# Kernel tuning notes

Measured on AMD Instinct MI355X. Metric: run time of the kernel, lower is better.

## Reference

```python
import jax, jax.numpy as jnp
import numpy as np

CLASS_NUM = 80
NUM_PRED = 2
TOPK = 1000
LEVEL_SIZES = [147456, 36864, 9216, 2304, 576]


def _make_anchors(key, n):
    k1, k2, k3, k4 = jax.random.split(key, 4)
    x1 = jax.random.uniform(k1, (n,)) * 1000.0
    y1 = jax.random.uniform(k2, (n,)) * 1000.0
    w = jax.random.uniform(k3, (n,)) * 200.0 + 8.0
    h = jax.random.uniform(k4, (n,)) * 200.0 + 8.0
    return jnp.stack([x1, y1, x1 + w, y1 + h], axis=1)


def setup_inputs() -> dict:
    key = jax.random.key(0)
    inp = {}
    for i, n in enumerate(LEVEL_SIZES):
        ka = jax.random.fold_in(key, 3 * i)
        kc = jax.random.fold_in(key, 3 * i + 1)
        kr = jax.random.fold_in(key, 3 * i + 2)
        inp[f"anchors{i}"] = _make_anchors(ka, n)
        inp[f"cls{i}"] = jax.random.normal(kc, (1, n, CLASS_NUM * NUM_PRED), dtype=jnp.float32)
        inp[f"reg{i}"] = jax.random.normal(kr, (1, n, 4 * NUM_PRED), dtype=jnp.float32) * 0.1
    return inp


def bbox_transform_inv(anchors, deltas):
    # anchors: [N,4] (x1,y1,x2,y2); deltas: [N,4] (dx,dy,dw,dh)
    w = anchors[:, 2] - anchors[:, 0] + 1.0
    h = anchors[:, 3] - anchors[:, 1] + 1.0
    cx = anchors[:, 0] + 0.5 * w
    cy = anchors[:, 1] + 0.5 * h
    pcx = cx + deltas[:, 0] * w
    pcy = cy + deltas[:, 1] * h
    pw = w * jnp.exp(deltas[:, 2])
    ph = h * jnp.exp(deltas[:, 3])
    return jnp.stack([pcx - 0.5 * pw, pcy - 0.5 * ph,
                      pcx + 0.5 * pw, pcy + 0.5 * ph], axis=1)


def _per_layer_inference(anchors_list, cls_list, reg_list):
    keep_a, keep_c, keep_r = [], [], []
    for a, c, r in zip(anchors_list, cls_list, reg_list):
        a = a.reshape(-1, 4)
        c = c[0].reshape(-1, CLASS_NUM * NUM_PRED)
        r = r[0].reshape(-1, 4 * NUM_PRED)
        if a.shape[0] > TOPK:
            ruler = jnp.max(c, axis=1)
            _, inds = jax.lax.top_k(ruler, TOPK)
            a, c, r = a[inds], c[inds], r[inds]
        keep_a.append(a)
        keep_c.append(jax.nn.sigmoid(c))
        keep_r.append(r)
    a = jnp.concatenate(keep_a, axis=0)   # [N,4]
    c = jnp.concatenate(keep_c, axis=0)   # [N, C*P]
    r = jnp.concatenate(keep_r, axis=0)   # [N, 4*P]
    n = a.shape[0]
    tag = (jnp.arange(CLASS_NUM, dtype=a.dtype) + 1.0)
    tag = jnp.tile(tag[None, :], (n, 1)).reshape(-1, 1)  # [N*C,1]
    scores0 = c[:, :CLASS_NUM].reshape(-1, 1)
    scores1 = c[:, CLASS_NUM:].reshape(-1, 1)
    bbox0 = bbox_transform_inv(a, r[:, :4])
    bbox1 = bbox_transform_inv(a, r[:, 4:])
    bbox0 = jnp.tile(bbox0, (1, CLASS_NUM)).reshape(-1, 4)
    bbox1 = jnp.tile(bbox1, (1, CLASS_NUM)).reshape(-1, 4)
    pred0 = jnp.concatenate([bbox0, scores0, tag], axis=1)
    pred1 = jnp.concatenate([bbox1, scores1, tag], axis=1)
    return jnp.concatenate([pred0, pred1], axis=1)  # [N*C, 12]


def reference(anchors0, anchors1, anchors2, anchors3, anchors4,
              cls0, cls1, cls2, cls3, cls4,
              reg0, reg1, reg2, reg3, reg4):
    return _per_layer_inference(
        [anchors0, anchors1, anchors2, anchors3, anchors4],
        [cls0, cls1, cls2, cls3, cls4],
        [reg0, reg1, reg2, reg3, reg4])
```

## Files before the change

kernel.cpp:

```cpp
#include <hip/hip_runtime.h>

#define CLS   160
#define TOPKN 1000
#define N0 147456
#define N1 36864
#define N2 9216
#define N3 2304
#define N4 576
#define NROWS (N0 + N1 + N2 + N3)
#define BD1 N0
#define BD2 (N0 + N1)
#define BD3 (N0 + N1 + N2)
#define NSEL (4 * TOPKN + N4)
#define NBINS 65536
#define CAND_CAP 2048

__device__ __forceinline__ unsigned sortable(float f) {
    unsigned u = __float_as_uint(f);
    return (u & 0x80000000u) ? ~u : (u | 0x80000000u);
}

__global__ __launch_bounds__(256) void k_ruler(
    const float* __restrict__ c0, const float* __restrict__ c1,
    const float* __restrict__ c2, const float* __restrict__ c3,
    unsigned* __restrict__ keys, unsigned* __restrict__ hist)
{
    int tid = blockIdx.x * 256 + threadIdx.x;
    if (tid < 4 * NBINS + 4096) hist[tid] = 0;

    int r0 = blockIdx.x << 7;
    const float* cb; int lr0;
    if (r0 < BD1)      { cb = c0; lr0 = r0; }
    else if (r0 < BD2) { cb = c1; lr0 = r0 - BD1; }
    else if (r0 < BD3) { cb = c2; lr0 = r0 - BD2; }
    else               { cb = c3; lr0 = r0 - BD3; }

    int wv   = threadIdx.x >> 6;
    int lane = threadIdx.x & 63;
    int sub  = lane >> 3;
    int col  = lane & 7;
    #pragma unroll
    for (int i = 0; i < 4; ++i) {
        int rrel = wv * 32 + i * 8 + sub;
        const float4* p = (const float4*)cb + (size_t)(lr0 + rrel) * 40 + col;
        float m = -3.4e38f;
        #pragma unroll
        for (int k = 0; k < 5; ++k) {
            float4 v = p[8 * k];
            m = fmaxf(m, fmaxf(fmaxf(v.x, v.y), fmaxf(v.z, v.w)));
        }
        m = fmaxf(m, __shfl_xor(m, 1));
        m = fmaxf(m, __shfl_xor(m, 2));
        m = fmaxf(m, __shfl_xor(m, 4));
        if (col == 0) keys[r0 + rrel] = sortable(m);
    }
}

__global__ __launch_bounds__(256) void k_hist(const unsigned* __restrict__ keys,
                                              unsigned* __restrict__ hist,
                                              unsigned* __restrict__ coarse)
{
    int b        = blockIdx.x;
    int level    = b >> 8;
    unsigned seg = (b >> 4) & 15;
    int chunk    = b & 15;
    __shared__ unsigned cnt[4096];
    for (int i = threadIdx.x; i < 4096; i += 256) cnt[i] = 0;
    __syncthreads();
    int base, n;
    switch (level) {
        case 0:  base = 0;   n = N0; break;
        case 1:  base = BD1; n = N1; break;
        case 2:  base = BD2; n = N2; break;
        default: base = BD3; n = N3; break;
    }
    int q = n >> 4;
    const uint4* kp = (const uint4*)(keys + base + chunk * q);
    int nv = q >> 2;
    for (int i = threadIdx.x; i < nv; i += 256) {
        uint4 k = kp[i];
        unsigned b0 = k.x >> 16, b1 = k.y >> 16, b2 = k.z >> 16, b3 = k.w >> 16;
        if ((b0 >> 12) == seg) atomicAdd(&cnt[b0 & 4095u], 1u);
        if ((b1 >> 12) == seg) atomicAdd(&cnt[b1 & 4095u], 1u);
        if ((b2 >> 12) == seg) atomicAdd(&cnt[b2 & 4095u], 1u);
        if ((b3 >> 12) == seg) atomicAdd(&cnt[b3 & 4095u], 1u);
    }
    __syncthreads();
    unsigned* h = hist + level * NBINS + (seg << 12);
    for (int i = threadIdx.x; i < 4096; i += 256) {
        unsigned c = cnt[i];
        if (c) atomicAdd(&h[i], c);
    }
    if (threadIdx.x < 64) {
        int j = threadIdx.x;
        unsigned s2 = 0;
        #pragma unroll 8
        for (int i = 0; i < 64; ++i) s2 += cnt[j * 64 + ((i + j) & 63)];
        if (s2) atomicAdd(&coarse[level * 1024 + (int)(seg << 6) + j], s2);
    }
}

__global__ __launch_bounds__(1024) void k_select(const unsigned* __restrict__ keys,
                                                 const unsigned* __restrict__ hist,
                                                 const unsigned* __restrict__ coarse,
                                                 unsigned* __restrict__ sel)
{
    int level = blockIdx.x;
    int t     = threadIdx.x;
    int lane  = t & 63;
    const unsigned* h = hist + level * NBINS;

    __shared__ unsigned s[1024];
    __shared__ unsigned long long a[CAND_CAP];
    __shared__ unsigned thr_s, cnt_s, chunk_s, cum0_s;

    s[t] = coarse[level * 1024 + t];
    if (t == 0) cnt_s = 0;
    __syncthreads();
    for (int off = 1; off < 1024; off <<= 1) {
        unsigned v   = s[t];
        unsigned add = (t + off < 1024) ? s[t + off] : 0u;
        __syncthreads();
        s[t] = v + add;
        __syncthreads();
    }
    if (s[t] >= TOPKN && (t == 1023 || s[t + 1] < TOPKN)) {
        chunk_s = (unsigned)t;
        cum0_s  = (t == 1023) ? 0u : s[t + 1];
    }
    __syncthreads();
    if (t < 64) {
        unsigned c = h[chunk_s * 64 + (unsigned)t];
        unsigned suf = c;
        #pragma unroll
        for (int off = 1; off < 64; off <<= 1) {
            unsigned v = __shfl_down(suf, off);
            if (t + off < 64) suf += v;
        }
        unsigned long long mask = __ballot(cum0_s + suf >= TOPKN);
        if (t == 0)
            thr_s = (chunk_s * 64 + (63 - (unsigned)__clzll(mask))) << 16;
    }
    __syncthreads();
    unsigned thr = thr_s;

    int base, n;
    switch (level) {
        case 0:  base = 0;   n = N0; break;
        case 1:  base = BD1; n = N1; break;
        case 2:  base = BD2; n = N2; break;
        default: base = BD3; n = N3; break;
    }
    const uint4* kp = (const uint4*)(keys + base);
    int nv = n >> 2;
    for (int i = t; i < nv; i += 1024) {
        uint4 k4 = kp[i];
        unsigned kv[4] = {k4.x, k4.y, k4.z, k4.w};
        #pragma unroll
        for (int c = 0; c < 4; ++c) {
            bool pass = kv[c] >= thr;
            unsigned long long mask = __ballot(pass);
            if (pass) {
                int leader    = __ffsll((long long)mask) - 1;
                unsigned tot  = (unsigned)__popcll(mask);
                unsigned rank = (unsigned)__popcll(mask & ((1ull << lane) - 1ull));
                unsigned bp = 0;
                if (lane == leader) bp = atomicAdd(&cnt_s, tot);
                bp = (unsigned)__shfl((int)bp, leader);
                unsigned pos = bp + rank;
                if (pos < CAND_CAP)
                    a[pos] = ((unsigned long long)kv[c] << 32) |
                             (unsigned)~(unsigned)(4 * i + c);
            }
        }
    }
    __syncthreads();
    unsigned cnt = cnt_s;
    if (cnt > CAND_CAP) cnt = CAND_CAP;

    for (int i = t; i < (int)cnt; i += 1024) {
        unsigned long long mine = a[i];
        unsigned rank = 0;
        for (int j = 0; j < (int)cnt; ++j) rank += (a[j] > mine) ? 1u : 0u;
        if (rank < TOPKN)
            sel[level * TOPKN + rank] = ~(unsigned)(mine & 0xFFFFFFFFull);
    }
}

__global__ __launch_bounds__(256) void k_epilogue(
    const float* a0, const float* a1, const float* a2, const float* a3, const float* a4,
    const float* c0, const float* c1, const float* c2, const float* c3, const float* c4,
    const float* r0, const float* r1, const float* r2, const float* r3, const float* r4,
    const unsigned* __restrict__ sel, float* __restrict__ out)
{
    int s = blockIdx.x;
    int level, idx;
    if (s < 4 * TOPKN) {
        level = s / TOPKN;
        idx   = (int)sel[s];
    } else {
        level = 4;
        idx   = s - 4 * TOPKN;
    }
    const float *A, *C, *R;
    switch (level) {
        case 0: A = a0; C = c0; R = r0; break;
        case 1: A = a1; C = c1; R = r1; break;
        case 2: A = a2; C = c2; R = r2; break;
        case 3: A = a3; C = c3; R = r3; break;
        default: A = a4; C = c4; R = r4; break;
    }

    __shared__ float sc[CLS];
    __shared__ float bb[8];

    const float* cp = C + (size_t)idx * CLS;
    if (threadIdx.x < CLS) {
        float x = cp[threadIdx.x];
        sc[threadIdx.x] = 1.0f / (1.0f + __expf(-x));
    }
    if (threadIdx.x == 192) {
        const float* ap = A + (size_t)idx * 4;
        const float* rp = R + (size_t)idx * 8;
        float x1 = ap[0], y1 = ap[1], x2 = ap[2], y2 = ap[3];
        float w  = x2 - x1 + 1.0f, h = y2 - y1 + 1.0f;
        float cx = x1 + 0.5f * w,  cy = y1 + 0.5f * h;
        #pragma unroll
        for (int p = 0; p < 2; ++p) {
            float pcx = cx + rp[4 * p + 0] * w;
            float pcy = cy + rp[4 * p + 1] * h;
            float pw  = w * __expf(rp[4 * p + 2]);
            float ph  = h * __expf(rp[4 * p + 3]);
            bb[4 * p + 0] = pcx - 0.5f * pw;
            bb[4 * p + 1] = pcy - 0.5f * ph;
            bb[4 * p + 2] = pcx + 0.5f * pw;
            bb[4 * p + 3] = pcy + 0.5f * ph;
        }
    }
    __syncthreads();

    float4* orow = (float4*)(out + (size_t)s * 960);
    if (threadIdx.x < 240) {
        int j = threadIdx.x / 3, part = threadIdx.x % 3;
        float tag = (float)(j + 1);
        float4 v;
        if (part == 0)      v = make_float4(bb[0], bb[1], bb[2], bb[3]);
        else if (part == 1) v = make_float4(sc[j], tag, bb[4], bb[5]);
        else                v = make_float4(bb[6], bb[7], sc[80 + j], tag);
        orow[threadIdx.x] = v;
    }
}

extern "C" void kernel_launch(void* const* d_in, const int* in_sizes, int n_in,
                              void* d_out, int out_size, void* d_ws, size_t ws_size,
                              hipStream_t stream)
{
    bool interleaved = (in_sizes[1] > 1000000);
    const float *A[5], *C[5], *R[5];
    for (int i = 0; i < 5; ++i) {
        if (interleaved) {
            A[i] = (const float*)d_in[3 * i + 0];
            C[i] = (const float*)d_in[3 * i + 1];
            R[i] = (const float*)d_in[3 * i + 2];
        } else {
            A[i] = (const float*)d_in[i];
            C[i] = (const float*)d_in[5 + i];
            R[i] = (const float*)d_in[10 + i];
        }
    }

    unsigned* keys   = (unsigned*)d_ws;
    unsigned* hist   = keys + NROWS;
    unsigned* coarse = hist + 4 * NBINS;
    unsigned* sel    = coarse + 4 * 1024;

    k_ruler<<<1530, 256, 0, stream>>>(C[0], C[1], C[2], C[3], keys, hist);
    k_hist<<<1024, 256, 0, stream>>>(keys, hist, coarse);
    k_select<<<4, 1024, 0, stream>>>(keys, hist, coarse, sel);
    k_epilogue<<<NSEL, 256, 0, stream>>>(A[0], A[1], A[2], A[3], A[4],
                                         C[0], C[1], C[2], C[3], C[4],
                                         R[0], R[1], R[2], R[3], R[4],
                                         sel, (float*)d_out);
}
```

Baseline: 82.41 us.

## Split top-k selection into parallel compaction and separate rank kernel

The single 4-block select kernel is split into a 64-block compaction kernel, with 16 slices per level that scan keys against the threshold and append candidates to global memory through global atomics, and a separate 4-block rank kernel. This spreads the key scan across more compute units instead of 4 blocks. In exchange it adds a kernel launch, global atomics and a global round trip for candidates. Each compaction block also recomputes the threshold scan redundantly.

```diff
diff --git a/kernel.cpp b/kernel.cpp
--- a/kernel.cpp
+++ b/kernel.cpp
@@ -26,7 +26,7 @@
     unsigned* __restrict__ keys, unsigned* __restrict__ hist)
 {
     int tid = blockIdx.x * 256 + threadIdx.x;
-    if (tid < 4 * NBINS + 4096) hist[tid] = 0;
+    if (tid < 4 * NBINS + 4096 + 8) hist[tid] = 0;
 
     int r0 = blockIdx.x << 7;
     const float* cb; int lr0;
@@ -100,22 +100,21 @@
     }
 }
 
-__global__ __launch_bounds__(1024) void k_select(const unsigned* __restrict__ keys,
-                                                 const unsigned* __restrict__ hist,
-                                                 const unsigned* __restrict__ coarse,
-                                                 unsigned* __restrict__ sel)
-{
-    int level = blockIdx.x;
+__global__ __launch_bounds__(1024) void k_compact(const unsigned* __restrict__ keys,
+                                                  const unsigned* __restrict__ hist,
+                                                  const unsigned* __restrict__ coarse,
+                                                  unsigned* __restrict__ ctrl,
+                                                  uint2* __restrict__ cand)
+{
+    int level = blockIdx.x >> 4;
+    int slice = blockIdx.x & 15;
     int t     = threadIdx.x;
     int lane  = t & 63;
-    const unsigned* h = hist + level * NBINS;
 
     __shared__ unsigned s[1024];
-    __shared__ unsigned long long a[CAND_CAP];
-    __shared__ unsigned thr_s, cnt_s, chunk_s, cum0_s;
+    __shared__ unsigned thr_s, chunk_s, cum0_s;
 
     s[t] = coarse[level * 1024 + t];
-    if (t == 0) cnt_s = 0;
     __syncthreads();
     for (int off = 1; off < 1024; off <<= 1) {
         unsigned v   = s[t];
@@ -130,29 +129,26 @@
     }
     __syncthreads();
     if (t < 64) {
+        const unsigned* h = hist + level * NBINS;
         unsigned c = h[chunk_s * 64 + (unsigned)t];
-        unsigned suf = c;
+        unsigned sufw = c;
         #pragma unroll
         for (int off = 1; off < 64; off <<= 1) {
-            unsigned v = __shfl_down(suf, off);
-            if (t + off < 64) suf += v;
-        }
-        unsigned long long mask = __ballot(cum0_s + suf >= TOPKN);
+            unsigned v = __shfl_down(sufw, off);
+            if (t + off < 64) sufw += v;
+        }
+        unsigned long long mask = __ballot(cum0_s + sufw >= TOPKN);
         if (t == 0)
             thr_s = (chunk_s * 64 + (63 - (unsigned)__clzll(mask))) << 16;
     }
     __syncthreads();
     unsigned thr = thr_s;
 
-    int base, n;
-    switch (level) {
-        case 0:  base = 0;   n = N0; break;
-        case 1:  base = BD1; n = N1; break;
-        case 2:  base = BD2; n = N2; break;
-        default: base = BD3; n = N3; break;
-    }
-    const uint4* kp = (const uint4*)(keys + base);
-    int nv = n >> 2;
+    int base = (level == 0) ? 0 : (level == 1) ? BD1 : (level == 2) ? BD2 : BD3;
+    int n    = (level == 0) ? N0 : (level == 1) ? N1 : (level == 2) ? N2 : N3;
+    int ns = n >> 4;
+    const uint4* kp = (const uint4*)(keys + base + slice * ns);
+    int nv = ns >> 2;
     for (int i = t; i < nv; i += 1024) {
         uint4 k4 = kp[i];
         unsigned kv[4] = {k4.x, k4.y, k4.z, k4.w};
@@ -165,20 +161,31 @@
                 unsigned tot  = (unsigned)__popcll(mask);
                 unsigned rank = (unsigned)__popcll(mask & ((1ull << lane) - 1ull));
                 unsigned bp = 0;
-                if (lane == leader) bp = atomicAdd(&cnt_s, tot);
+                if (lane == leader) bp = atomicAdd(&ctrl[4 + level], tot);
                 bp = (unsigned)__shfl((int)bp, leader);
                 unsigned pos = bp + rank;
                 if (pos < CAND_CAP)
-                    a[pos] = ((unsigned long long)kv[c] << 32) |
-                             (unsigned)~(unsigned)(4 * i + c);
+                    cand[level * CAND_CAP + pos] =
+                        make_uint2(kv[c], (unsigned)(slice * ns + 4 * i + c));
             }
         }
     }
-    __syncthreads();
-    unsigned cnt = cnt_s;
+}
+
+__global__ __launch_bounds__(1024) void k_rank(const uint2* __restrict__ cand,
+                                               const unsigned* __restrict__ ctrl,
+                                               unsigned* __restrict__ sel)
+{
+    int level = blockIdx.x;
+    unsigned cnt = ctrl[4 + level];
     if (cnt > CAND_CAP) cnt = CAND_CAP;
-
-    for (int i = t; i < (int)cnt; i += 1024) {
+    __shared__ unsigned long long a[CAND_CAP];
+    for (int i = threadIdx.x; i < (int)cnt; i += 1024) {
+        uint2 c = cand[level * CAND_CAP + i];
+        a[i] = ((unsigned long long)c.x << 32) | (unsigned)(~c.y);
+    }
+    __syncthreads();
+    for (int i = threadIdx.x; i < (int)cnt; i += 1024) {
         unsigned long long mine = a[i];
         unsigned rank = 0;
         for (int j = 0; j < (int)cnt; ++j) rank += (a[j] > mine) ? 1u : 0u;
@@ -272,11 +279,14 @@
     unsigned* keys   = (unsigned*)d_ws;
     unsigned* hist   = keys + NROWS;
     unsigned* coarse = hist + 4 * NBINS;
-    unsigned* sel    = coarse + 4 * 1024;
+    unsigned* ctrl   = coarse + 4096;
+    uint2*    cand   = (uint2*)(ctrl + 8);
+    unsigned* sel    = (unsigned*)(cand + 4 * CAND_CAP);
 
     k_ruler<<<1530, 256, 0, stream>>>(C[0], C[1], C[2], C[3], keys, hist);
     k_hist<<<1024, 256, 0, stream>>>(keys, hist, coarse);
-    k_select<<<4, 1024, 0, stream>>>(keys, hist, coarse, sel);
+    k_compact<<<64, 1024, 0, stream>>>(keys, hist, coarse, ctrl, cand);
+    k_rank<<<4, 1024, 0, stream>>>(cand, ctrl, sel);
     k_epilogue<<<NSEL, 256, 0, stream>>>(A[0], A[1], A[2], A[3], A[4],
                                          C[0], C[1], C[2], C[3], C[4],
                                          R[0], R[1], R[2], R[3], R[4],
```

New measurement: 90.08 us. 1.09x slower.

## Fuse histogram, select and epilogue into one persistent kernel with grid barriers

Applied to the files above, without the earlier changes.

Replaces the histogram, select and epilogue kernels with a single 64-block persistent kernel. Blocks keep their key slice in registers, build a 10-bit coarse histogram with wave-aggregated atomics, then refine only the winning coarse bin, so the large 64K-bin histogram and its zeroing are gone. Candidate selection is spread across 16 slices per level and cross-block progress uses spin-wait counters in global memory. The level-4 and top-k epilogue rows are handled by four teams inside each block. The aim is to cut launch overhead and the cost of the large histogram, in exchange for less parallelism in the epilogue, grid-barrier spin latency, and a reliance on all 64 blocks being resident at once.

```diff
diff --git a/kernel.cpp b/kernel.cpp
--- a/kernel.cpp
+++ b/kernel.cpp
@@ -12,8 +12,21 @@
 #define BD2 (N0 + N1)
 #define BD3 (N0 + N1 + N2)
 #define NSEL (4 * TOPKN + N4)
-#define NBINS 65536
 #define CAND_CAP 2048
+#define KMAX 9
+
+struct KP {
+    const float *A0, *A1, *A2, *A3, *A4;
+    const float *C0, *C1, *C2, *C3, *C4;
+    const float *R0, *R1, *R2, *R3, *R4;
+    unsigned *keys;
+    unsigned *coarse;
+    unsigned *fine_g;
+    unsigned *ctl;
+    unsigned long long *cand;
+    unsigned *sel;
+    float *out;
+};
 
 __device__ __forceinline__ unsigned sortable(float f) {
     unsigned u = __float_as_uint(f);
@@ -23,10 +36,10 @@
 __global__ __launch_bounds__(256) void k_ruler(
     const float* __restrict__ c0, const float* __restrict__ c1,
     const float* __restrict__ c2, const float* __restrict__ c3,
-    unsigned* __restrict__ keys, unsigned* __restrict__ hist)
+    unsigned* __restrict__ keys, unsigned* __restrict__ zbuf)
 {
     int tid = blockIdx.x * 256 + threadIdx.x;
-    if (tid < 4 * NBINS + 4096) hist[tid] = 0;
+    if (tid < 4480) zbuf[tid] = 0;
 
     int r0 = blockIdx.x << 7;
     const float* cb; int lr0;
@@ -56,66 +69,106 @@
     }
 }
 
-__global__ __launch_bounds__(256) void k_hist(const unsigned* __restrict__ keys,
-                                              unsigned* __restrict__ hist,
-                                              unsigned* __restrict__ coarse)
+__global__ __launch_bounds__(1024) void k_mega(KP p)
 {
-    int b        = blockIdx.x;
-    int level    = b >> 8;
-    unsigned seg = (b >> 4) & 15;
-    int chunk    = b & 15;
-    __shared__ unsigned cnt[4096];
-    for (int i = threadIdx.x; i < 4096; i += 256) cnt[i] = 0;
-    __syncthreads();
-    int base, n;
-    switch (level) {
-        case 0:  base = 0;   n = N0; break;
-        case 1:  base = BD1; n = N1; break;
-        case 2:  base = BD2; n = N2; break;
-        default: base = BD3; n = N3; break;
-    }
-    int q = n >> 4;
-    const uint4* kp = (const uint4*)(keys + base + chunk * q);
-    int nv = q >> 2;
-    for (int i = threadIdx.x; i < nv; i += 256) {
-        uint4 k = kp[i];
-        unsigned b0 = k.x >> 16, b1 = k.y >> 16, b2 = k.z >> 16, b3 = k.w >> 16;
-        if ((b0 >> 12) == seg) atomicAdd(&cnt[b0 & 4095u], 1u);
-        if ((b1 >> 12) == seg) atomicAdd(&cnt[b1 & 4095u], 1u);
-        if ((b2 >> 12) == seg) atomicAdd(&cnt[b2 & 4095u], 1u);
-        if ((b3 >> 12) == seg) atomicAdd(&cnt[b3 & 4095u], 1u);
-    }
-    __syncthreads();
-    unsigned* h = hist + level * NBINS + (seg << 12);
-    for (int i = threadIdx.x; i < 4096; i += 256) {
-        unsigned c = cnt[i];
-        if (c) atomicAdd(&h[i], c);
-    }
-    if (threadIdx.x < 64) {
-        int j = threadIdx.x;
-        unsigned s2 = 0;
-        #pragma unroll 8
-        for (int i = 0; i < 64; ++i) s2 += cnt[j * 64 + ((i + j) & 63)];
-        if (s2) atomicAdd(&coarse[level * 1024 + (int)(seg << 6) + j], s2);
-    }
-}
-
-__global__ __launch_bounds__(1024) void k_select(const unsigned* __restrict__ keys,
-                                                 const unsigned* __restrict__ hist,
-                                                 const unsigned* __restrict__ coarse,
-                                                 unsigned* __restrict__ sel)
-{
-    int level = blockIdx.x;
-    int t     = threadIdx.x;
-    int lane  = t & 63;
-    const unsigned* h = hist + level * NBINS;
+    const int b = blockIdx.x, lvl = b >> 4, slice = b & 15;
+    const int t = threadIdx.x, lane = t & 63;
+    const int team = t >> 8, tt = t & 255;
 
     __shared__ unsigned s[1024];
+    __shared__ unsigned fine[64];
     __shared__ unsigned long long a[CAND_CAP];
-    __shared__ unsigned thr_s, cnt_s, chunk_s, cum0_s;
-
-    s[t] = coarse[level * 1024 + t];
-    if (t == 0) cnt_s = 0;
+    __shared__ float sc[4][CLS];
+    __shared__ float bbx[4][8];
+    __shared__ unsigned thr_s, blockcnt, gbase_s, Cstar_s, cum0_s;
+
+    const int lbase = (lvl == 0) ? 0 : (lvl == 1) ? BD1 : (lvl == 2) ? BD2 : BD3;
+    const int ln    = (lvl == 0) ? N0 : (lvl == 1) ? N1 : (lvl == 2) ? N2 : N3;
+    const int ns    = ln >> 4;
+    const unsigned* kp = p.keys + lbase + slice * ns;
+
+    unsigned* done1 = p.ctl + 0;
+    unsigned* done2 = p.ctl + 4;
+    unsigned* done3 = p.ctl + 8;
+    unsigned* done4 = p.ctl + 12;
+    unsigned* cntp  = p.ctl + 32 + 16 * lvl;
+
+    s[t] = 0;
+    if (t == 0) blockcnt = 0;
+    __syncthreads();
+
+    unsigned kreg[KMAX];
+    #pragma unroll
+    for (int j = 0; j < KMAX; ++j) {
+        int li = j * 1024 + t;
+        kreg[j] = (li < ns) ? kp[li] : 0u;
+    }
+    #pragma unroll
+    for (int j = 0; j < KMAX; ++j) {
+        int li = j * 1024 + t;
+        bool valid = li < ns;
+        unsigned ch = kreg[j] >> 22;
+        unsigned long long todo = __ballot(valid);
+        while (todo) {
+            int leader = __ffsll((long long)todo) - 1;
+            unsigned chl = (unsigned)__shfl((int)ch, leader);
+            unsigned long long m = __ballot(valid && (ch == chl));
+            if (lane == leader) atomicAdd(&s[chl], (unsigned)__popcll(m));
+            todo &= ~m;
+        }
+    }
+    __syncthreads();
+    { unsigned c = s[t]; if (c) atomicAdd(&p.coarse[lvl * 1024 + t], c); }
+
+    #pragma unroll
+    for (int k = 0; k < 3; ++k) {
+        int r4 = b + 64 * (team + 4 * k);
+        bool act = r4 < N4;
+        if (act) {
+            const float* cp = p.C4 + (size_t)r4 * CLS;
+            if (tt < CLS) sc[team][tt] = 1.0f / (1.0f + __expf(-cp[tt]));
+            if (tt == 192) {
+                const float* ap = p.A4 + (size_t)r4 * 4;
+                const float* rp = p.R4 + (size_t)r4 * 8;
+                float x1 = ap[0], y1 = ap[1], x2 = ap[2], y2 = ap[3];
+                float w = x2 - x1 + 1.0f, h = y2 - y1 + 1.0f;
+                float cx = x1 + 0.5f * w, cy = y1 + 0.5f * h;
+                #pragma unroll
+                for (int q = 0; q < 2; ++q) {
+                    float pcx = cx + rp[4 * q + 0] * w;
+                    float pcy = cy + rp[4 * q + 1] * h;
+                    float pw  = w * __expf(rp[4 * q + 2]);
+                    float ph  = h * __expf(rp[4 * q + 3]);
+                    bbx[team][4 * q + 0] = pcx - 0.5f * pw;
+                    bbx[team][4 * q + 1] = pcy - 0.5f * ph;
+                    bbx[team][4 * q + 2] = pcx + 0.5f * pw;
+                    bbx[team][4 * q + 3] = pcy + 0.5f * ph;
+                }
+            }
+        }
+        __syncthreads();
+        if (act && tt < 240) {
+            float4* orow = (float4*)(p.out + (size_t)(4 * TOPKN + r4) * 960);
+            int j = tt / 3, part = tt % 3;
+            float tag = (float)(j + 1);
+            float4 v;
+            if (part == 0)      v = make_float4(bbx[team][0], bbx[team][1], bbx[team][2], bbx[team][3]);
+            else if (part == 1) v = make_float4(sc[team][j], tag, bbx[team][4], bbx[team][5]);
+            else                v = make_float4(bbx[team][6], bbx[team][7], sc[team][80 + j], tag);
+            orow[tt] = v;
+        }
+        __syncthreads();
+    }
+
+    __syncthreads();
+    if (t == 0) {
+        __threadfence(); atomicAdd(&done1[lvl], 1u);
+        while (atomicAdd(&done1[lvl], 0u) < 16u) __builtin_amdgcn_s_sleep(2);
+        __threadfence();
+    }
+    __syncthreads();
+
+    s[t] = p.coarse[lvl * 1024 + t];
     __syncthreads();
     for (int off = 1; off < 1024; off <<= 1) {
         unsigned v   = s[t];
@@ -125,12 +178,33 @@
         __syncthreads();
     }
     if (s[t] >= TOPKN && (t == 1023 || s[t + 1] < TOPKN)) {
-        chunk_s = (unsigned)t;
+        Cstar_s = (unsigned)t;
         cum0_s  = (t == 1023) ? 0u : s[t + 1];
     }
     __syncthreads();
+    unsigned Cstar = Cstar_s;
+
+    if (t < 64) fine[t] = 0;
+    __syncthreads();
+    #pragma unroll
+    for (int j = 0; j < KMAX; ++j) {
+        int li = j * 1024 + t;
+        if (li < ns && (kreg[j] >> 22) == Cstar)
+            atomicAdd(&fine[(kreg[j] >> 16) & 63u], 1u);
+    }
+    __syncthreads();
+    if (t < 64 && fine[t]) atomicAdd(&p.fine_g[lvl * 64 + t], fine[t]);
+
+    __syncthreads();
+    if (t == 0) {
+        __threadfence(); atomicAdd(&done2[lvl], 1u);
+        while (atomicAdd(&done2[lvl], 0u) < 16u) __builtin_amdgcn_s_sleep(2);
+        __threadfence();
+    }
+    __syncthreads();
+
     if (t < 64) {
-        unsigned c = h[chunk_s * 64 + (unsigned)t];
+        unsigned c = p.fine_g[lvl * 64 + t];
         unsigned suf = c;
         #pragma unroll
         for (int off = 1; off < 64; off <<= 1) {
@@ -139,115 +213,109 @@
         }
         unsigned long long mask = __ballot(cum0_s + suf >= TOPKN);
         if (t == 0)
-            thr_s = (chunk_s * 64 + (63 - (unsigned)__clzll(mask))) << 16;
+            thr_s = ((Cstar << 6) + (63u - (unsigned)__clzll(mask))) << 16;
     }
     __syncthreads();
     unsigned thr = thr_s;
 
-    int base, n;
-    switch (level) {
-        case 0:  base = 0;   n = N0; break;
-        case 1:  base = BD1; n = N1; break;
-        case 2:  base = BD2; n = N2; break;
-        default: base = BD3; n = N3; break;
-    }
-    const uint4* kp = (const uint4*)(keys + base);
-    int nv = n >> 2;
-    for (int i = t; i < nv; i += 1024) {
-        uint4 k4 = kp[i];
-        unsigned kv[4] = {k4.x, k4.y, k4.z, k4.w};
-        #pragma unroll
-        for (int c = 0; c < 4; ++c) {
-            bool pass = kv[c] >= thr;
-            unsigned long long mask = __ballot(pass);
-            if (pass) {
-                int leader    = __ffsll((long long)mask) - 1;
-                unsigned tot  = (unsigned)__popcll(mask);
-                unsigned rank = (unsigned)__popcll(mask & ((1ull << lane) - 1ull));
-                unsigned bp = 0;
-                if (lane == leader) bp = atomicAdd(&cnt_s, tot);
-                bp = (unsigned)__shfl((int)bp, leader);
-                unsigned pos = bp + rank;
-                if (pos < CAND_CAP)
-                    a[pos] = ((unsigned long long)kv[c] << 32) |
-                             (unsigned)~(unsigned)(4 * i + c);
+    #pragma unroll
+    for (int j = 0; j < KMAX; ++j) {
+        int li = j * 1024 + t;
+        bool pass = (li < ns) && (kreg[j] >= thr);
+        unsigned long long mask = __ballot(pass);
+        if (pass) {
+            int leader   = __ffsll((long long)mask) - 1;
+            unsigned tot = (unsigned)__popcll(mask);
+            unsigned rk  = (unsigned)__popcll(mask & ((1ull << lane) - 1ull));
+            unsigned wb = 0;
+            if (lane == leader) wb = atomicAdd(&blockcnt, tot);
+            wb = (unsigned)__shfl((int)wb, leader);
+            unsigned pos = wb + rk;
+            if (pos < CAND_CAP)
+                a[pos] = ((unsigned long long)kreg[j] << 32) |
+                         (unsigned)~(unsigned)(slice * ns + li);
+        }
+    }
+    __syncthreads();
+    unsigned bc = blockcnt; if (bc > CAND_CAP) bc = CAND_CAP;
+    if (t == 0) gbase_s = atomicAdd(cntp, bc);
+    __syncthreads();
+    unsigned gb = gbase_s;
+    for (unsigned i = t; i < bc; i += 1024)
+        if (gb + i < CAND_CAP) p.cand[lvl * CAND_CAP + gb + i] = a[i];
+
+    __syncthreads();
+    if (t == 0) {
+        __threadfence(); atomicAdd(&done3[lvl], 1u);
+        while (atomicAdd(&done3[lvl], 0u) < 16u) __builtin_amdgcn_s_sleep(2);
+        __threadfence();
+    }
+    __syncthreads();
+
+    if (slice == 0) {
+        unsigned cntv = atomicAdd(cntp, 0u);
+        if (cntv > CAND_CAP) cntv = CAND_CAP;
+        for (unsigned i = t; i < cntv; i += 1024) a[i] = p.cand[lvl * CAND_CAP + i];
+        __syncthreads();
+        for (unsigned i = t; i < cntv; i += 1024) {
+            unsigned long long mine = a[i];
+            unsigned rank = 0;
+            for (unsigned j2 = 0; j2 < cntv; ++j2) rank += (a[j2] > mine) ? 1u : 0u;
+            if (rank < TOPKN)
+                p.sel[lvl * TOPKN + rank] = ~(unsigned)(mine & 0xFFFFFFFFull);
+        }
+        __syncthreads();
+        if (t == 0) { __threadfence(); atomicAdd(&done4[lvl], 1u); }
+    }
+
+    if (t == 0) {
+        while (atomicAdd(&done4[lvl], 0u) < 1u) __builtin_amdgcn_s_sleep(2);
+        __threadfence();
+    }
+    __syncthreads();
+
+    const float *A = (lvl == 0) ? p.A0 : (lvl == 1) ? p.A1 : (lvl == 2) ? p.A2 : p.A3;
+    const float *C = (lvl == 0) ? p.C0 : (lvl == 1) ? p.C1 : (lvl == 2) ? p.C2 : p.C3;
+    const float *R = (lvl == 0) ? p.R0 : (lvl == 1) ? p.R1 : (lvl == 2) ? p.R2 : p.R3;
+    for (int k = 0; k < 16; ++k) {
+        int r = slice + 16 * team + 64 * k;
+        bool act = r < TOPKN;
+        int sidx = lvl * TOPKN + r;
+        if (act) {
+            int idx = (int)p.sel[sidx];
+            const float* cp = C + (size_t)idx * CLS;
+            if (tt < CLS) sc[team][tt] = 1.0f / (1.0f + __expf(-cp[tt]));
+            if (tt == 192) {
+                const float* ap = A + (size_t)idx * 4;
+                const float* rp = R + (size_t)idx * 8;
+                float x1 = ap[0], y1 = ap[1], x2 = ap[2], y2 = ap[3];
+                float w = x2 - x1 + 1.0f, h = y2 - y1 + 1.0f;
+                float cx = x1 + 0.5f * w, cy = y1 + 0.5f * h;
+                #pragma unroll
+                for (int q = 0; q < 2; ++q) {
+                    float pcx = cx + rp[4 * q + 0] * w;
+                    float pcy = cy + rp[4 * q + 1] * h;
+                    float pw  = w * __expf(rp[4 * q + 2]);
+                    float ph  = h * __expf(rp[4 * q + 3]);
+                    bbx[team][4 * q + 0] = pcx - 0.5f * pw;
+                    bbx[team][4 * q + 1] = pcy - 0.5f * ph;
+                    bbx[team][4 * q + 2] = pcx + 0.5f * pw;
+                    bbx[team][4 * q + 3] = pcy + 0.5f * ph;
+                }
             }
         }
-    }
-    __syncthreads();
-    unsigned cnt = cnt_s;
-    if (cnt > CAND_CAP) cnt = CAND_CAP;
-
-    for (int i = t; i < (int)cnt; i += 1024) {
-        unsigned long long mine = a[i];
-        unsigned rank = 0;
-        for (int j = 0; j < (int)cnt; ++j) rank += (a[j] > mine) ? 1u : 0u;
-        if (rank < TOPKN)
-            sel[level * TOPKN + rank] = ~(unsigned)(mine & 0xFFFFFFFFull);
-    }
-}
-
-__global__ __launch_bounds__(256) void k_epilogue(
-    const float* a0, const float* a1, const float* a2, const float* a3, const float* a4,
-    const float* c0, const float* c1, const float* c2, const float* c3, const float* c4,
-    const float* r0, const float* r1, const float* r2, const float* r3, const float* r4,
-    const unsigned* __restrict__ sel, float* __restrict__ out)
-{
-    int s = blockIdx.x;
-    int level, idx;
-    if (s < 4 * TOPKN) {
-        level = s / TOPKN;
-        idx   = (int)sel[s];
-    } else {
-        level = 4;
-        idx   = s - 4 * TOPKN;
-    }
-    const float *A, *C, *R;
-    switch (level) {
-        case 0: A = a0; C = c0; R = r0; break;
-        case 1: A = a1; C = c1; R = r1; break;
-        case 2: A = a2; C = c2; R = r2; break;
-        case 3: A = a3; C = c3; R = r3; break;
-        default: A = a4; C = c4; R = r4; break;
-    }
-
-    __shared__ float sc[CLS];
-    __shared__ float bb[8];
-
-    const float* cp = C + (size_t)idx * CLS;
-    if (threadIdx.x < CLS) {
-        float x = cp[threadIdx.x];
-        sc[threadIdx.x] = 1.0f / (1.0f + __expf(-x));
-    }
-    if (threadIdx.x == 192) {
-        const float* ap = A + (size_t)idx * 4;
-        const float* rp = R + (size_t)idx * 8;
-        float x1 = ap[0], y1 = ap[1], x2 = ap[2], y2 = ap[3];
-        float w  = x2 - x1 + 1.0f, h = y2 - y1 + 1.0f;
-        float cx = x1 + 0.5f * w,  cy = y1 + 0.5f * h;
-        #pragma unroll
-        for (int p = 0; p < 2; ++p) {
-            float pcx = cx + rp[4 * p + 0] * w;
-            float pcy = cy + rp[4 * p + 1] * h;
-            float pw  = w * __expf(rp[4 * p + 2]);
-            float ph  = h * __expf(rp[4 * p + 3]);
-            bb[4 * p + 0] = pcx - 0.5f * pw;
-            bb[4 * p + 1] = pcy - 0.5f * ph;
-            bb[4 * p + 2] = pcx + 0.5f * pw;
-            bb[4 * p + 3] = pcy + 0.5f * ph;
-        }
-    }
-    __syncthreads();
-
-    float4* orow = (float4*)(out + (size_t)s * 960);
-    if (threadIdx.x < 240) {
-        int j = threadIdx.x / 3, part = threadIdx.x % 3;
-        float tag = (float)(j + 1);
-        float4 v;
-        if (part == 0)      v = make_float4(bb[0], bb[1], bb[2], bb[3]);
-        else if (part == 1) v = make_float4(sc[j], tag, bb[4], bb[5]);
-        else                v = make_float4(bb[6], bb[7], sc[80 + j], tag);
-        orow[threadIdx.x] = v;
+        __syncthreads();
+        if (act && tt < 240) {
+            float4* orow = (float4*)(p.out + (size_t)sidx * 960);
+            int j = tt / 3, part = tt % 3;
+            float tag = (float)(j + 1);
+            float4 v;
+            if (part == 0)      v = make_float4(bbx[team][0], bbx[team][1], bbx[team][2], bbx[team][3]);
+            else if (part == 1) v = make_float4(sc[team][j], tag, bbx[team][4], bbx[team][5]);
+            else                v = make_float4(bbx[team][6], bbx[team][7], sc[team][80 + j], tag);
+            orow[tt] = v;
+        }
+        __syncthreads();
     }
 }
 
@@ -270,15 +338,19 @@
     }
 
     unsigned* keys   = (unsigned*)d_ws;
-    unsigned* hist   = keys + NROWS;
-    unsigned* coarse = hist + 4 * NBINS;
-    unsigned* sel    = coarse + 4 * 1024;
-
-    k_ruler<<<1530, 256, 0, stream>>>(C[0], C[1], C[2], C[3], keys, hist);
-    k_hist<<<1024, 256, 0, stream>>>(keys, hist, coarse);
-    k_select<<<4, 1024, 0, stream>>>(keys, hist, coarse, sel);
-    k_epilogue<<<NSEL, 256, 0, stream>>>(A[0], A[1], A[2], A[3], A[4],
-                                         C[0], C[1], C[2], C[3], C[4],
-                                         R[0], R[1], R[2], R[3], R[4],
-                                         sel, (float*)d_out);
+    unsigned* coarse = keys + NROWS;
+    unsigned* fine_g = coarse + 4 * 1024;
+    unsigned* ctl    = fine_g + 4 * 64;
+    unsigned long long* cand = (unsigned long long*)(ctl + 128);
+    unsigned* sel    = (unsigned*)(cand + 4 * CAND_CAP);
+
+    KP p;
+    p.A0 = A[0]; p.A1 = A[1]; p.A2 = A[2]; p.A3 = A[3]; p.A4 = A[4];
+    p.C0 = C[0]; p.C1 = C[1]; p.C2 = C[2]; p.C3 = C[3]; p.C4 = C[4];
+    p.R0 = R[0]; p.R1 = R[1]; p.R2 = R[2]; p.R3 = R[3]; p.R4 = R[4];
+    p.keys = keys; p.coarse = coarse; p.fine_g = fine_g; p.ctl = ctl;
+    p.cand = cand; p.sel = sel; p.out = (float*)d_out;
+
+    k_ruler<<<1530, 256, 0, stream>>>(C[0], C[1], C[2], C[3], keys, coarse);
+    k_mega<<<64, 1024, 0, stream>>>(p);
 }
```

Result: slower. 98.89 us (+20.0%).

## Move level-4 epilogue into ruler kernel and replace atomic compaction with prefix scan

Applied to the files above, without the earlier changes.

The 576 rows of level 4 need no top-k, so their output rows are now written by extra blocks of the ruler kernel instead of the final epilogue launch, which shrinks the epilogue grid to 4000 blocks. In the select kernel, candidate compaction no longer does a ballot plus shared atomic for every key. Each thread buffers up to 16 passing keys in registers, and a block-wide prefix scan assigns write offsets. The risk is that a thread with more than 16 passing keys silently drops candidates, and the scan adds many barriers.

```diff
diff --git a/kernel.cpp b/kernel.cpp
--- a/kernel.cpp
+++ b/kernel.cpp
@@ -11,215 +11,25 @@
 #define BD1 N0
 #define BD2 (N0 + N1)
 #define BD3 (N0 + N1 + N2)
-#define NSEL (4 * TOPKN + N4)
 #define NBINS 65536
 #define CAND_CAP 2048
+#define PMAX 16
 
 __device__ __forceinline__ unsigned sortable(float f) {
     unsigned u = __float_as_uint(f);
     return (u & 0x80000000u) ? ~u : (u | 0x80000000u);
 }
 
-__global__ __launch_bounds__(256) void k_ruler(
-    const float* __restrict__ c0, const float* __restrict__ c1,
-    const float* __restrict__ c2, const float* __restrict__ c3,
-    unsigned* __restrict__ keys, unsigned* __restrict__ hist)
-{
-    int tid = blockIdx.x * 256 + threadIdx.x;
-    if (tid < 4 * NBINS + 4096) hist[tid] = 0;
-
-    int r0 = blockIdx.x << 7;
-    const float* cb; int lr0;
-    if (r0 < BD1)      { cb = c0; lr0 = r0; }
-    else if (r0 < BD2) { cb = c1; lr0 = r0 - BD1; }
-    else if (r0 < BD3) { cb = c2; lr0 = r0 - BD2; }
-    else               { cb = c3; lr0 = r0 - BD3; }
-
-    int wv   = threadIdx.x >> 6;
-    int lane = threadIdx.x & 63;
-    int sub  = lane >> 3;
-    int col  = lane & 7;
-    #pragma unroll
-    for (int i = 0; i < 4; ++i) {
-        int rrel = wv * 32 + i * 8 + sub;
-        const float4* p = (const float4*)cb + (size_t)(lr0 + rrel) * 40 + col;
-        float m = -3.4e38f;
-        #pragma unroll
-        for (int k = 0; k < 5; ++k) {
-            float4 v = p[8 * k];
-            m = fmaxf(m, fmaxf(fmaxf(v.x, v.y), fmaxf(v.z, v.w)));
-        }
-        m = fmaxf(m, __shfl_xor(m, 1));
-        m = fmaxf(m, __shfl_xor(m, 2));
-        m = fmaxf(m, __shfl_xor(m, 4));
-        if (col == 0) keys[r0 + rrel] = sortable(m);
-    }
-}
-
-__global__ __launch_bounds__(256) void k_hist(const unsigned* __restrict__ keys,
-                                              unsigned* __restrict__ hist,
-                                              unsigned* __restrict__ coarse)
-{
-    int b        = blockIdx.x;
-    int level    = b >> 8;
-    unsigned seg = (b >> 4) & 15;
-    int chunk    = b & 15;
-    __shared__ unsigned cnt[4096];
-    for (int i = threadIdx.x; i < 4096; i += 256) cnt[i] = 0;
-    __syncthreads();
-    int base, n;
-    switch (level) {
-        case 0:  base = 0;   n = N0; break;
-        case 1:  base = BD1; n = N1; break;
-        case 2:  base = BD2; n = N2; break;
-        default: base = BD3; n = N3; break;
-    }
-    int q = n >> 4;
-    const uint4* kp = (const uint4*)(keys + base + chunk * q);
-    int nv = q >> 2;
-    for (int i = threadIdx.x; i < nv; i += 256) {
-        uint4 k = kp[i];
-        unsigned b0 = k.x >> 16, b1 = k.y >> 16, b2 = k.z >> 16, b3 = k.w >> 16;
-        if ((b0 >> 12) == seg) atomicAdd(&cnt[b0 & 4095u], 1u);
-        if ((b1 >> 12) == seg) atomicAdd(&cnt[b1 & 4095u], 1u);
-        if ((b2 >> 12) == seg) atomicAdd(&cnt[b2 & 4095u], 1u);
-        if ((b3 >> 12) == seg) atomicAdd(&cnt[b3 & 4095u], 1u);
-    }
-    __syncthreads();
-    unsigned* h = hist + level * NBINS + (seg << 12);
-    for (int i = threadIdx.x; i < 4096; i += 256) {
-        unsigned c = cnt[i];
-        if (c) atomicAdd(&h[i], c);
-    }
-    if (threadIdx.x < 64) {
-        int j = threadIdx.x;
-        unsigned s2 = 0;
-        #pragma unroll 8
-        for (int i = 0; i < 64; ++i) s2 += cnt[j * 64 + ((i + j) & 63)];
-        if (s2) atomicAdd(&coarse[level * 1024 + (int)(seg << 6) + j], s2);
-    }
-}
-
-__global__ __launch_bounds__(1024) void k_select(const unsigned* __restrict__ keys,
-                                                 const unsigned* __restrict__ hist,
-                                                 const unsigned* __restrict__ coarse,
-                                                 unsigned* __restrict__ sel)
-{
-    int level = blockIdx.x;
-    int t     = threadIdx.x;
-    int lane  = t & 63;
-    const unsigned* h = hist + level * NBINS;
-
-    __shared__ unsigned s[1024];
-    __shared__ unsigned long long a[CAND_CAP];
-    __shared__ unsigned thr_s, cnt_s, chunk_s, cum0_s;
-
-    s[t] = coarse[level * 1024 + t];
-    if (t == 0) cnt_s = 0;
-    __syncthreads();
-    for (int off = 1; off < 1024; off <<= 1) {
-        unsigned v   = s[t];
-        unsigned add = (t + off < 1024) ? s[t + off] : 0u;
-        __syncthreads();
-        s[t] = v + add;
-        __syncthreads();
-    }
-    if (s[t] >= TOPKN && (t == 1023 || s[t + 1] < TOPKN)) {
-        chunk_s = (unsigned)t;
-        cum0_s  = (t == 1023) ? 0u : s[t + 1];
-    }
-    __syncthreads();
-    if (t < 64) {
-        unsigned c = h[chunk_s * 64 + (unsigned)t];
-        unsigned suf = c;
-        #pragma unroll
-        for (int off = 1; off < 64; off <<= 1) {
-            unsigned v = __shfl_down(suf, off);
-            if (t + off < 64) suf += v;
-        }
-        unsigned long long mask = __ballot(cum0_s + suf >= TOPKN);
-        if (t == 0)
-            thr_s = (chunk_s * 64 + (63 - (unsigned)__clzll(mask))) << 16;
-    }
-    __syncthreads();
-    unsigned thr = thr_s;
-
-    int base, n;
-    switch (level) {
-        case 0:  base = 0;   n = N0; break;
-        case 1:  base = BD1; n = N1; break;
-        case 2:  base = BD2; n = N2; break;
-        default: base = BD3; n = N3; break;
-    }
-    const uint4* kp = (const uint4*)(keys + base);
-    int nv = n >> 2;
-    for (int i = t; i < nv; i += 1024) {
-        uint4 k4 = kp[i];
-        unsigned kv[4] = {k4.x, k4.y, k4.z, k4.w};
-        #pragma unroll
-        for (int c = 0; c < 4; ++c) {
-            bool pass = kv[c] >= thr;
-            unsigned long long mask = __ballot(pass);
-            if (pass) {
-                int leader    = __ffsll((long long)mask) - 1;
-                unsigned tot  = (unsigned)__popcll(mask);
-                unsigned rank = (unsigned)__popcll(mask & ((1ull << lane) - 1ull));
-                unsigned bp = 0;
-                if (lane == leader) bp = atomicAdd(&cnt_s, tot);
-                bp = (unsigned)__shfl((int)bp, leader);
-                unsigned pos = bp + rank;
-                if (pos < CAND_CAP)
-                    a[pos] = ((unsigned long long)kv[c] << 32) |
-                             (unsigned)~(unsigned)(4 * i + c);
-            }
-        }
-    }
-    __syncthreads();
-    unsigned cnt = cnt_s;
-    if (cnt > CAND_CAP) cnt = CAND_CAP;
-
-    for (int i = t; i < (int)cnt; i += 1024) {
-        unsigned long long mine = a[i];
-        unsigned rank = 0;
-        for (int j = 0; j < (int)cnt; ++j) rank += (a[j] > mine) ? 1u : 0u;
-        if (rank < TOPKN)
-            sel[level * TOPKN + rank] = ~(unsigned)(mine & 0xFFFFFFFFull);
-    }
-}
-
-__global__ __launch_bounds__(256) void k_epilogue(
-    const float* a0, const float* a1, const float* a2, const float* a3, const float* a4,
-    const float* c0, const float* c1, const float* c2, const float* c3, const float* c4,
-    const float* r0, const float* r1, const float* r2, const float* r3, const float* r4,
-    const unsigned* __restrict__ sel, float* __restrict__ out)
-{
-    int s = blockIdx.x;
-    int level, idx;
-    if (s < 4 * TOPKN) {
-        level = s / TOPKN;
-        idx   = (int)sel[s];
-    } else {
-        level = 4;
-        idx   = s - 4 * TOPKN;
-    }
-    const float *A, *C, *R;
-    switch (level) {
-        case 0: A = a0; C = c0; R = r0; break;
-        case 1: A = a1; C = c1; R = r1; break;
-        case 2: A = a2; C = c2; R = r2; break;
-        case 3: A = a3; C = c3; R = r3; break;
-        default: A = a4; C = c4; R = r4; break;
-    }
-
-    __shared__ float sc[CLS];
-    __shared__ float bb[8];
-
+__device__ __forceinline__ void epilogue_row(
+    const float* A, const float* C, const float* R, int idx, int s,
+    float* out, float* sc, float* bb, int tt)
+{
     const float* cp = C + (size_t)idx * CLS;
-    if (threadIdx.x < CLS) {
-        float x = cp[threadIdx.x];
-        sc[threadIdx.x] = 1.0f / (1.0f + __expf(-x));
-    }
-    if (threadIdx.x == 192) {
+    if (tt < CLS) {
+        float x = cp[tt];
+        sc[tt] = 1.0f / (1.0f + __expf(-x));
+    }
+    if (tt == 192) {
         const float* ap = A + (size_t)idx * 4;
         const float* rp = R + (size_t)idx * 8;
         float x1 = ap[0], y1 = ap[1], x2 = ap[2], y2 = ap[3];
@@ -238,17 +48,212 @@
         }
     }
     __syncthreads();
-
     float4* orow = (float4*)(out + (size_t)s * 960);
-    if (threadIdx.x < 240) {
-        int j = threadIdx.x / 3, part = threadIdx.x % 3;
+    if (tt < 240) {
+        int j = tt / 3, part = tt % 3;
         float tag = (float)(j + 1);
         float4 v;
         if (part == 0)      v = make_float4(bb[0], bb[1], bb[2], bb[3]);
         else if (part == 1) v = make_float4(sc[j], tag, bb[4], bb[5]);
         else                v = make_float4(bb[6], bb[7], sc[80 + j], tag);
-        orow[threadIdx.x] = v;
-    }
+        orow[tt] = v;
+    }
+}
+
+__global__ __launch_bounds__(256) void k_ruler(
+    const float* __restrict__ c0, const float* __restrict__ c1,
+    const float* __restrict__ c2, const float* __restrict__ c3,
+    const float* __restrict__ a4, const float* __restrict__ c4,
+    const float* __restrict__ r4,
+    unsigned* __restrict__ keys, unsigned* __restrict__ hist,
+    float* __restrict__ out)
+{
+    int tid = blockIdx.x * 256 + threadIdx.x;
+    if (tid < 4 * NBINS + 4096) hist[tid] = 0;
+
+    if (blockIdx.x >= 1530) {
+        __shared__ float sc[CLS];
+        __shared__ float bb[8];
+        int s4 = blockIdx.x - 1530;
+        epilogue_row(a4, c4, r4, s4, 4 * TOPKN + s4, out, sc, bb, threadIdx.x);
+        return;
+    }
+
+    int r0 = blockIdx.x << 7;
+    const float* cb; int lr0;
+    if (r0 < BD1)      { cb = c0; lr0 = r0; }
+    else if (r0 < BD2) { cb = c1; lr0 = r0 - BD1; }
+    else if (r0 < BD3) { cb = c2; lr0 = r0 - BD2; }
+    else               { cb = c3; lr0 = r0 - BD3; }
+
+    int wv   = threadIdx.x >> 6;
+    int lane = threadIdx.x & 63;
+    int sub  = lane >> 3;
+    int col  = lane & 7;
+    #pragma unroll
+    for (int i = 0; i < 4; ++i) {
+        int rrel = wv * 32 + i * 8 + sub;
+        const float4* p = (const float4*)cb + (size_t)(lr0 + rrel) * 40 + col;
+        float m = -3.4e38f;
+        #pragma unroll
+        for (int k = 0; k < 5; ++k) {
+            float4 v = p[8 * k];
+            m = fmaxf(m, fmaxf(fmaxf(v.x, v.y), fmaxf(v.z, v.w)));
+        }
+        m = fmaxf(m, __shfl_xor(m, 1));
+        m = fmaxf(m, __shfl_xor(m, 2));
+        m = fmaxf(m, __shfl_xor(m, 4));
+        if (col == 0) keys[r0 + rrel] = sortable(m);
+    }
+}
+
+__global__ __launch_bounds__(256) void k_hist(const unsigned* __restrict__ keys,
+                                              unsigned* __restrict__ hist,
+                                              unsigned* __restrict__ coarse)
+{
+    int b        = blockIdx.x;
+    int level    = b >> 8;
+    unsigned seg = (b >> 4) & 15;
+    int chunk    = b & 15;
+    __shared__ unsigned cnt[4096];
+    for (int i = threadIdx.x; i < 4096; i += 256) cnt[i] = 0;
+    __syncthreads();
+    int base, n;
+    switch (level) {
+        case 0:  base = 0;   n = N0; break;
+        case 1:  base = BD1; n = N1; break;
+        case 2:  base = BD2; n = N2; break;
+        default: base = BD3; n = N3; break;
+    }
+    int q = n >> 4;
+    const uint4* kp = (const uint4*)(keys + base + chunk * q);
+    int nv = q >> 2;
+    for (int i = threadIdx.x; i < nv; i += 256) {
+        uint4 k = kp[i];
+        unsigned b0 = k.x >> 16, b1 = k.y >> 16, b2 = k.z >> 16, b3 = k.w >> 16;
+        if ((b0 >> 12) == seg) atomicAdd(&cnt[b0 & 4095u], 1u);
+        if ((b1 >> 12) == seg) atomicAdd(&cnt[b1 & 4095u], 1u);
+        if ((b2 >> 12) == seg) atomicAdd(&cnt[b2 & 4095u], 1u);
+        if ((b3 >> 12) == seg) atomicAdd(&cnt[b3 & 4095u], 1u);
+    }
+    __syncthreads();
+    unsigned* h = hist + level * NBINS + (seg << 12);
+    for (int i = threadIdx.x; i < 4096; i += 256) {
+        unsigned c = cnt[i];
+        if (c) atomicAdd(&h[i], c);
+    }
+    if (threadIdx.x < 64) {
+        int j = threadIdx.x;
+        unsigned s2 = 0;
+        #pragma unroll 8
+        for (int i = 0; i < 64; ++i) s2 += cnt[j * 64 + ((i + j) & 63)];
+        if (s2) atomicAdd(&coarse[level * 1024 + (int)(seg << 6) + j], s2);
+    }
+}
+
+__global__ __launch_bounds__(1024) void k_select(const unsigned* __restrict__ keys,
+                                                 const unsigned* __restrict__ hist,
+                                                 const unsigned* __restrict__ coarse,
+                                                 unsigned* __restrict__ sel)
+{
+    int level = blockIdx.x;
+    int t     = threadIdx.x;
+
+    __shared__ unsigned s[1024];
+    __shared__ unsigned long long a[CAND_CAP];
+    __shared__ unsigned thr_s, chunk_s, cum0_s;
+
+    s[t] = coarse[level * 1024 + t];
+    __syncthreads();
+    for (int off = 1; off < 1024; off <<= 1) {
+        unsigned v   = s[t];
+        unsigned add = (t + off < 1024) ? s[t + off] : 0u;
+        __syncthreads();
+        s[t] = v + add;
+        __syncthreads();
+    }
+    if (s[t] >= TOPKN && (t == 1023 || s[t + 1] < TOPKN)) {
+        chunk_s = (unsigned)t;
+        cum0_s  = (t == 1023) ? 0u : s[t + 1];
+    }
+    __syncthreads();
+    if (t < 64) {
+        const unsigned* h = hist + level * NBINS;
+        unsigned c = h[chunk_s * 64 + (unsigned)t];
+        unsigned suf = c;
+        #pragma unroll
+        for (int off = 1; off < 64; off <<= 1) {
+            unsigned v = __shfl_down(suf, off);
+            if (t + off < 64) suf += v;
+        }
+        unsigned long long mask = __ballot(cum0_s + suf >= TOPKN);
+        if (t == 0)
+            thr_s = ((chunk_s << 6) + (63u - (unsigned)__clzll(mask))) << 16;
+    }
+    __syncthreads();
+    unsigned thr = thr_s;
+
+    int base = (level == 0) ? 0 : (level == 1) ? BD1 : (level == 2) ? BD2 : BD3;
+    int n    = (level == 0) ? N0 : (level == 1) ? N1 : (level == 2) ? N2 : N3;
+    const uint4* kp = (const uint4*)(keys + base);
+    int nv = n >> 2;
+    unsigned pk[PMAX], pidx[PMAX];
+    int pc = 0;
+    for (int i = t; i < nv; i += 1024) {
+        uint4 k4 = kp[i];
+        if (k4.x >= thr && pc < PMAX) { pk[pc] = k4.x; pidx[pc] = 4 * i + 0; ++pc; }
+        if (k4.y >= thr && pc < PMAX) { pk[pc] = k4.y; pidx[pc] = 4 * i + 1; ++pc; }
+        if (k4.z >= thr && pc < PMAX) { pk[pc] = k4.z; pidx[pc] = 4 * i + 2; ++pc; }
+        if (k4.w >= thr && pc < PMAX) { pk[pc] = k4.w; pidx[pc] = 4 * i + 3; ++pc; }
+    }
+    __syncthreads();
+    s[t] = (unsigned)pc;
+    __syncthreads();
+    for (int off = 1; off < 1024; off <<= 1) {
+        unsigned v   = s[t];
+        unsigned add = (t >= off) ? s[t - off] : 0u;
+        __syncthreads();
+        s[t] = v + add;
+        __syncthreads();
+    }
+    unsigned my_base = s[t] - (unsigned)pc;
+    unsigned cnt = s[1023];
+    if (cnt > CAND_CAP) cnt = CAND_CAP;
+    for (int j = 0; j < pc; ++j) {
+        unsigned pos = my_base + (unsigned)j;
+        if (pos < CAND_CAP)
+            a[pos] = ((unsigned long long)pk[j] << 32) | (unsigned)~pidx[j];
+    }
+    __syncthreads();
+
+    for (int i = t; i < (int)cnt; i += 1024) {
+        unsigned long long mine = a[i];
+        unsigned rank = 0;
+        for (int j = 0; j < (int)cnt; ++j) rank += (a[j] > mine) ? 1u : 0u;
+        if (rank < TOPKN)
+            sel[level * TOPKN + rank] = ~(unsigned)(mine & 0xFFFFFFFFull);
+    }
+}
+
+__global__ __launch_bounds__(256) void k_epilogue(
+    const float* a0, const float* a1, const float* a2, const float* a3,
+    const float* c0, const float* c1, const float* c2, const float* c3,
+    const float* r0, const float* r1, const float* r2, const float* r3,
+    const unsigned* __restrict__ sel, float* __restrict__ out)
+{
+    int s = blockIdx.x;
+    int level = s / TOPKN;
+    int idx   = (int)sel[s];
+    const float *A, *C, *R;
+    switch (level) {
+        case 0: A = a0; C = c0; R = r0; break;
+        case 1: A = a1; C = c1; R = r1; break;
+        case 2: A = a2; C = c2; R = r2; break;
+        default: A = a3; C = c3; R = r3; break;
+    }
+    __shared__ float sc[CLS];
+    __shared__ float bb[8];
+    epilogue_row(A, C, R, idx, s, out, sc, bb, threadIdx.x);
 }
 
 extern "C" void kernel_launch(void* const* d_in, const int* in_sizes, int n_in,
@@ -272,13 +277,15 @@
     unsigned* keys   = (unsigned*)d_ws;
     unsigned* hist   = keys + NROWS;
     unsigned* coarse = hist + 4 * NBINS;
-    unsigned* sel    = coarse + 4 * 1024;
-
-    k_ruler<<<1530, 256, 0, stream>>>(C[0], C[1], C[2], C[3], keys, hist);
+    unsigned* sel    = coarse + 4096;
+
+    k_ruler<<<2106, 256, 0, stream>>>(C[0], C[1], C[2], C[3],
+                                      A[4], C[4], R[4],
+                                      keys, hist, (float*)d_out);
     k_hist<<<1024, 256, 0, stream>>>(keys, hist, coarse);
     k_select<<<4, 1024, 0, stream>>>(keys, hist, coarse, sel);
-    k_epilogue<<<NSEL, 256, 0, stream>>>(A[0], A[1], A[2], A[3], A[4],
-                                         C[0], C[1], C[2], C[3], C[4],
-                                         R[0], R[1], R[2], R[3], R[4],
-                                         sel, (float*)d_out);
-}
+    k_epilogue<<<4 * TOPKN, 256, 0, stream>>>(A[0], A[1], A[2], A[3],
+                                              C[0], C[1], C[2], C[3],
+                                              R[0], R[1], R[2], R[3],
+                                              sel, (float*)d_out);
+}
```

New measurement: 95.74 us. +16.2%, slower.
